# Optimization experiments

Hardware: AMD Instinct MI355X
Metric: run time of the kernel (lower is better)

Reference implementation:

```python
import jax, jax.numpy as jnp
import numpy as np

B, C, N, D = 8, 64, 512, 64

def setup_inputs() -> dict:
    key = jax.random.key(0)
    k1, = jax.random.split(key, 1)
    inp = jax.random.normal(k1, (B, C, N, D), dtype=jnp.float32)
    a = jnp.full((1, C, 1, 1), 0.75, dtype=jnp.float32)
    b = jnp.full((1, C, 1, 1), 0.25, dtype=jnp.float32)
    return {"inp": inp, "a": a, "b": b}

def reference(inp, a, b):
    # A = inp @ inp^T : [B, C, N, N]
    A = jnp.einsum('bcnd,bcmd->bcnm', inp, inp)
    # B = A @ A : [B, C, N, N]
    B2 = jnp.einsum('bcnk,bckm->bcnm', A, A)
    Mat = -a * A + b * B2
    # out = inp + Mat @ inp : [B, C, N, D]
    out = inp + jnp.einsum('bcnm,bcmd->bcnd', Mat, inp)
    return out
```

## Files before the change

### kernel.cpp

```cpp
#include <hip/hip_runtime.h>


typedef __bf16 bf16;
typedef __attribute__((ext_vector_type(8)))  __bf16 bf16x8;
typedef __attribute__((ext_vector_type(4)))  __bf16 bf16x4;
typedef __attribute__((ext_vector_type(16))) float  f32x16;

namespace {

constexpr int DD = 64;

__device__ __forceinline__ int sxz(int d) { return ((d >> 1) ^ (d >> 4)) & 7; }

__global__ __launch_bounds__(512, 4)
void ns_mfma(const float* __restrict__ inp, const float* __restrict__ aw,
             const float* __restrict__ bw, float* __restrict__ out) {
    __shared__ unsigned char smem[54272] __attribute__((aligned(128)));
    bf16*  const Xt0 = (bf16*)smem;
    bf16*  const Xt1 = (bf16*)(smem + 9216);
    bf16*  const Xr  = (bf16*)smem;
    float* const Gp  = (float*)(smem + 18432);
    bf16*  const Gbf = (bf16*)(smem + 35840);
    bf16*  const Hbf = (bf16*)(smem + 45056);

    const int slice = blockIdx.x;
    const float av = aw[slice & 63];
    const float bv = bw[slice & 63];
    const float* __restrict__ X = inp + (size_t)slice * (512 * DD);
    float* __restrict__ O       = out + (size_t)slice * (512 * DD);

    const int t    = threadIdx.x;
    const int lane = t & 63;
    const int w    = t >> 6;
    const int l31  = lane & 31;
    const int l5   = lane >> 5;
    const int half = t >> 8;
    const int th   = t & 255;
    const int s_nq = th >> 4;
    const int s_dq = th & 15;

    bf16x4 xr[4][4];
    {
        float4 rv[4][4];
#pragma unroll
        for (int s = 0; s < 4; ++s)
#pragma unroll
            for (int rn = 0; rn < 4; ++rn)
                rv[s][rn] = *(const float4*)&X[(256 * half + 64 * s + 4 * s_nq + rn) * DD + 4 * s_dq];
#pragma unroll
        for (int s = 0; s < 4; ++s)
#pragma unroll
            for (int rn = 0; rn < 4; ++rn) {
                xr[s][rn][0] = (bf16)rv[s][rn].x;
                xr[s][rn][1] = (bf16)rv[s][rn].y;
                xr[s][rn][2] = (bf16)rv[s][rn].z;
                xr[s][rn][3] = (bf16)rv[s][rn].w;
            }
    }

    f32x16 acc;
#pragma unroll
    for (int q = 0; q < 16; ++q) acc[q] = 0.f;

    bf16* const XtMine = half ? Xt1 : Xt0;
    const int tile = w & 3;
    const int i32  = (tile >> 1) * 32;
    const int j32  = (tile & 1) * 32;
    const int rowA = i32 + l31;
    const int rowB = j32 + l31;
    const int sA   = sxz(rowA);
    const int sB   = sxz(rowB);

    for (int it = 0; it < 4; ++it) {
#pragma unroll
        for (int r = 0; r < 4; ++r) {
            const int d = 4 * s_dq + r;
            bf16x4 v;
            v[0] = xr[it][0][r]; v[1] = xr[it][1][r];
            v[2] = xr[it][2][r]; v[3] = xr[it][3][r];
            const int g = ((s_nq >> 1) ^ sxz(d)) & 7;
            *(bf16x4*)&XtMine[d * 72 + g * 8 + 4 * (s_nq & 1)] = v;
        }
        __syncthreads();
#pragma unroll
        for (int ks = 0; ks < 4; ++ks) {
            const int gw = 2 * ks + l5;
            bf16x8 a = *(const bf16x8*)&XtMine[rowA * 72 + ((gw ^ sA) & 7) * 8];
            bf16x8 b = *(const bf16x8*)&XtMine[rowB * 72 + ((gw ^ sB) & 7) * 8];
            acc = __builtin_amdgcn_mfma_f32_32x32x16_bf16(a, b, acc, 0, 0, 0);
        }
        __syncthreads();
    }

    if (half == 0) {
#pragma unroll
        for (int q = 0; q < 16; ++q) {
            const int r = (q & 3) + 8 * (q >> 2) + 4 * l5;
            Gp[(i32 + r) * 68 + j32 + l31] = acc[q];
        }
    }
    __syncthreads();
    if (half == 1) {
#pragma unroll
        for (int q = 0; q < 16; ++q) {
            const int r  = (q & 3) + 8 * (q >> 2) + 4 * l5;
            const int ii = i32 + r;
            const int jj = j32 + l31;
            Gbf[ii * 72 + jj] = (bf16)(acc[q] + Gp[ii * 68 + jj]);
        }
    }
    __syncthreads();

    if (w < 4) {
        const int pi = (w >> 1) * 32;
        const int pj = (w & 1) * 32;
        f32x16 h;
#pragma unroll
        for (int q = 0; q < 16; ++q) h[q] = 0.f;
#pragma unroll
        for (int ks = 0; ks < 4; ++ks) {
            bf16x8 a = *(const bf16x8*)&Gbf[(pi + l31) * 72 + ks * 16 + 8 * l5];
            bf16x8 b = *(const bf16x8*)&Gbf[(pj + l31) * 72 + ks * 16 + 8 * l5];
            h = __builtin_amdgcn_mfma_f32_32x32x16_bf16(a, b, h, 0, 0, 0);
        }
#pragma unroll
        for (int q = 0; q < 16; ++q) {
            const int r  = (q & 3) + 8 * (q >> 2) + 4 * l5;
            const int ii = pi + r;
            const int jj = pj + l31;
            Hbf[ii * 72 + jj] = (bf16)(bv * h[q] - av * (float)Gbf[ii * 72 + jj]);
        }
    }
    __syncthreads();

    const int nb = (w >> 1) * 32;
    const int db = (w & 1) * 32;

    for (int it = 0; it < 4; ++it) {
        if (half == (it >> 1)) {
#pragma unroll
            for (int ss = 0; ss < 2; ++ss) {
                const int s   = 2 * (it & 1) + ss;
                const int nlb = 64 * ss + 4 * s_nq;
#pragma unroll
                for (int rn = 0; rn < 4; ++rn)
                    *(bf16x4*)&Xr[(nlb + rn) * 72 + 4 * s_dq] = xr[s][rn];
            }
        }
        __syncthreads();

        f32x16 o;
#pragma unroll
        for (int q = 0; q < 16; ++q) o[q] = 0.f;
#pragma unroll
        for (int ks = 0; ks < 4; ++ks) {
            bf16x8 a = *(const bf16x8*)&Xr [(nb + l31) * 72 + ks * 16 + 8 * l5];
            bf16x8 b = *(const bf16x8*)&Hbf[(db + l31) * 72 + ks * 16 + 8 * l5];
            o = __builtin_amdgcn_mfma_f32_32x32x16_bf16(a, b, o, 0, 0, 0);
        }

#pragma unroll
        for (int q = 0; q < 16; ++q) {
            const int rl = (q & 3) + 8 * (q >> 2) + 4 * l5;
            const int nl = nb + rl;
            const int d  = db + l31;
            O[(size_t)(it * 128 + nl) * DD + d] = o[q] + (float)Xr[nl * 72 + d];
        }
        __syncthreads();
    }
}

}

extern "C" void kernel_launch(void* const* d_in, const int* in_sizes, int n_in,
                              void* d_out, int out_size, void* d_ws, size_t ws_size,
                              hipStream_t stream) {
    const float* inp = (const float*)d_in[0];
    const float* aw  = (const float*)d_in[1];
    const float* bw  = (const float*)d_in[2];
    float* out       = (float*)d_out;

    ns_mfma<<<dim3(512), dim3(512), 0, stream>>>(inp, aw, bw, out);
}
```

Measured before the change: 25.61 us.

## Stream input chunks with double-buffered prefetch and reorder row ownership

Input rows are now loaded 128 at a time, with the next chunk prefetched into a two-slot float4 buffer while the current chunk is converted to bf16 and fed to the Gram MFMA loop. This replaces the upfront load of all 16 float4 per thread. Row ownership changes so both thread halves contribute to every 128-row chunk. The first output chunk is staged into shared memory during the Gram reduction, and one barrier per output iteration is removed. The goal is to overlap global-load latency with compute and lower peak register use, at the cost of more interleaved load and barrier logic.

```diff
diff --git a/kernel.cpp b/kernel.cpp
--- a/kernel.cpp
+++ b/kernel.cpp
@@ -7,8 +7,6 @@
 typedef __attribute__((ext_vector_type(16))) float  f32x16;
 
 namespace {
-
-constexpr int DD = 64;
 
 __device__ __forceinline__ int sxz(int d) { return ((d >> 1) ^ (d >> 4)) & 7; }
 
@@ -24,10 +22,8 @@
     bf16*  const Hbf = (bf16*)(smem + 45056);
 
     const int slice = blockIdx.x;
-    const float av = aw[slice & 63];
-    const float bv = bw[slice & 63];
-    const float* __restrict__ X = inp + (size_t)slice * (512 * DD);
-    float* __restrict__ O       = out + (size_t)slice * (512 * DD);
+    const float* __restrict__ X = inp + (size_t)slice * (512 * 64);
+    float* __restrict__ O       = out + (size_t)slice * (512 * 64);
 
     const int t    = threadIdx.x;
     const int lane = t & 63;
@@ -39,24 +35,16 @@
     const int s_nq = th >> 4;
     const int s_dq = th & 15;
 
-    bf16x4 xr[4][4];
-    {
-        float4 rv[4][4];
+    const float* __restrict__ Xbase =
+        X + (size_t)(64 * half + 4 * s_nq) * 64 + 4 * s_dq;
+
+    float4 rv[2][4];
 #pragma unroll
-        for (int s = 0; s < 4; ++s)
-#pragma unroll
-            for (int rn = 0; rn < 4; ++rn)
-                rv[s][rn] = *(const float4*)&X[(256 * half + 64 * s + 4 * s_nq + rn) * DD + 4 * s_dq];
-#pragma unroll
-        for (int s = 0; s < 4; ++s)
-#pragma unroll
-            for (int rn = 0; rn < 4; ++rn) {
-                xr[s][rn][0] = (bf16)rv[s][rn].x;
-                xr[s][rn][1] = (bf16)rv[s][rn].y;
-                xr[s][rn][2] = (bf16)rv[s][rn].z;
-                xr[s][rn][3] = (bf16)rv[s][rn].w;
-            }
-    }
+    for (int rn = 0; rn < 4; ++rn)
+        rv[0][rn] = *(const float4*)&Xbase[(size_t)rn * 64];
+
+    const float av = aw[slice & 63];
+    const float bv = bw[slice & 63];
 
     f32x16 acc;
 #pragma unroll
@@ -71,7 +59,22 @@
     const int sA   = sxz(rowA);
     const int sB   = sxz(rowB);
 
+    bf16x4 xr[4][4];
+
+#pragma unroll
     for (int it = 0; it < 4; ++it) {
+        if (it < 3) {
+#pragma unroll
+            for (int rn = 0; rn < 4; ++rn)
+                rv[(it + 1) & 1][rn] =
+                    *(const float4*)&Xbase[(size_t)(128 * (it + 1) + rn) * 64];
+        }
+#pragma unroll
+        for (int rn = 0; rn < 4; ++rn) {
+            const float4 v = rv[it & 1][rn];
+            xr[it][rn][0] = (bf16)v.x; xr[it][rn][1] = (bf16)v.y;
+            xr[it][rn][2] = (bf16)v.z; xr[it][rn][3] = (bf16)v.w;
+        }
 #pragma unroll
         for (int r = 0; r < 4; ++r) {
             const int d = 4 * s_dq + r;
@@ -99,6 +102,9 @@
             Gp[(i32 + r) * 68 + j32 + l31] = acc[q];
         }
     }
+#pragma unroll
+    for (int rn = 0; rn < 4; ++rn)
+        *(bf16x4*)&Xr[(64 * half + 4 * s_nq + rn) * 72 + 4 * s_dq] = xr[0][rn];
     __syncthreads();
     if (half == 1) {
 #pragma unroll
@@ -136,19 +142,8 @@
     const int nb = (w >> 1) * 32;
     const int db = (w & 1) * 32;
 
+#pragma unroll
     for (int it = 0; it < 4; ++it) {
-        if (half == (it >> 1)) {
-#pragma unroll
-            for (int ss = 0; ss < 2; ++ss) {
-                const int s   = 2 * (it & 1) + ss;
-                const int nlb = 64 * ss + 4 * s_nq;
-#pragma unroll
-                for (int rn = 0; rn < 4; ++rn)
-                    *(bf16x4*)&Xr[(nlb + rn) * 72 + 4 * s_dq] = xr[s][rn];
-            }
-        }
-        __syncthreads();
-
         f32x16 o;
 #pragma unroll
         for (int q = 0; q < 16; ++q) o[q] = 0.f;
@@ -158,15 +153,20 @@
             bf16x8 b = *(const bf16x8*)&Hbf[(db + l31) * 72 + ks * 16 + 8 * l5];
             o = __builtin_amdgcn_mfma_f32_32x32x16_bf16(a, b, o, 0, 0, 0);
         }
-
 #pragma unroll
         for (int q = 0; q < 16; ++q) {
             const int rl = (q & 3) + 8 * (q >> 2) + 4 * l5;
             const int nl = nb + rl;
             const int d  = db + l31;
-            O[(size_t)(it * 128 + nl) * DD + d] = o[q] + (float)Xr[nl * 72 + d];
+            O[(size_t)(it * 128 + nl) * 64 + d] = o[q] + (float)Xr[nl * 72 + d];
         }
-        __syncthreads();
+        if (it < 3) {
+            __syncthreads();
+#pragma unroll
+            for (int rn = 0; rn < 4; ++rn)
+                *(bf16x4*)&Xr[(64 * half + 4 * s_nq + rn) * 72 + 4 * s_dq] = xr[it + 1][rn];
+            __syncthreads();
+        }
     }
 }
 
```

Result: slower. 26.57 us (+3.8%).

## Double-buffer LDS staging tiles to halve barriers in Gram and output phases

Applied to the files above, without the earlier changes.

Each half of the block now gets two ping-pong LDS buffers for its transposed X tile, which removes the trailing barrier in each Gram accumulation step. The half assignment is inverted so the half holding the first 256 rows stages its row-major X tiles into two Xr buffers while the other half writes its partial Gram. The output loop then alternates between Xr0 and Xr1, filling the next buffer while the current one is consumed, with one barrier per step instead of two. In exchange, shared memory grows to about 71 KB and the launch-bounds occupancy hint drops from 4 to 2, which gives the compiler more registers but may lower residency.

```diff
diff --git a/kernel.cpp b/kernel.cpp
--- a/kernel.cpp
+++ b/kernel.cpp
@@ -8,26 +8,21 @@
 
 namespace {
 
-constexpr int DD = 64;
-
 __device__ __forceinline__ int sxz(int d) { return ((d >> 1) ^ (d >> 4)) & 7; }
 
-__global__ __launch_bounds__(512, 4)
+__global__ __launch_bounds__(512, 2)
 void ns_mfma(const float* __restrict__ inp, const float* __restrict__ aw,
              const float* __restrict__ bw, float* __restrict__ out) {
-    __shared__ unsigned char smem[54272] __attribute__((aligned(128)));
-    bf16*  const Xt0 = (bf16*)smem;
-    bf16*  const Xt1 = (bf16*)(smem + 9216);
-    bf16*  const Xr  = (bf16*)smem;
-    float* const Gp  = (float*)(smem + 18432);
-    bf16*  const Gbf = (bf16*)(smem + 35840);
-    bf16*  const Hbf = (bf16*)(smem + 45056);
+    __shared__ unsigned char smem[72704] __attribute__((aligned(128)));
+    float* const Gp  = (float*)(smem + 36864);
+    bf16*  const Gbf = (bf16*)(smem + 54272);
+    bf16*  const Hbf = (bf16*)(smem + 63488);
+    bf16*  const Xr0 = (bf16*)smem;
+    bf16*  const Xr1 = (bf16*)(smem + 18432);
 
     const int slice = blockIdx.x;
-    const float av = aw[slice & 63];
-    const float bv = bw[slice & 63];
-    const float* __restrict__ X = inp + (size_t)slice * (512 * DD);
-    float* __restrict__ O       = out + (size_t)slice * (512 * DD);
+    const float* __restrict__ X = inp + (size_t)slice * 32768;
+    float* __restrict__ O       = out + (size_t)slice * 32768;
 
     const int t    = threadIdx.x;
     const int lane = t & 63;
@@ -39,6 +34,9 @@
     const int s_nq = th >> 4;
     const int s_dq = th & 15;
 
+    const float* __restrict__ Xbase =
+        X + (size_t)(256 * (1 - half) + 4 * s_nq) * 64 + 4 * s_dq;
+
     bf16x4 xr[4][4];
     {
         float4 rv[4][4];
@@ -46,7 +44,7 @@
         for (int s = 0; s < 4; ++s)
 #pragma unroll
             for (int rn = 0; rn < 4; ++rn)
-                rv[s][rn] = *(const float4*)&X[(256 * half + 64 * s + 4 * s_nq + rn) * DD + 4 * s_dq];
+                rv[s][rn] = *(const float4*)&Xbase[(size_t)(64 * s + rn) * 64];
 #pragma unroll
         for (int s = 0; s < 4; ++s)
 #pragma unroll
@@ -57,12 +55,13 @@
                 xr[s][rn][3] = (bf16)rv[s][rn].w;
             }
     }
+    const float av = aw[slice & 63];
+    const float bv = bw[slice & 63];
 
     f32x16 acc;
 #pragma unroll
     for (int q = 0; q < 16; ++q) acc[q] = 0.f;
 
-    bf16* const XtMine = half ? Xt1 : Xt0;
     const int tile = w & 3;
     const int i32  = (tile >> 1) * 32;
     const int j32  = (tile & 1) * 32;
@@ -71,7 +70,11 @@
     const int sA   = sxz(rowA);
     const int sB   = sxz(rowB);
 
+    unsigned char* const XtH = smem + half * 18432;
+
+#pragma unroll
     for (int it = 0; it < 4; ++it) {
+        bf16* const Xt = (bf16*)(XtH + (it & 1) * 9216);
 #pragma unroll
         for (int r = 0; r < 4; ++r) {
             const int d = 4 * s_dq + r;
@@ -79,24 +82,33 @@
             v[0] = xr[it][0][r]; v[1] = xr[it][1][r];
             v[2] = xr[it][2][r]; v[3] = xr[it][3][r];
             const int g = ((s_nq >> 1) ^ sxz(d)) & 7;
-            *(bf16x4*)&XtMine[d * 72 + g * 8 + 4 * (s_nq & 1)] = v;
+            *(bf16x4*)&Xt[d * 72 + g * 8 + 4 * (s_nq & 1)] = v;
         }
         __syncthreads();
 #pragma unroll
         for (int ks = 0; ks < 4; ++ks) {
             const int gw = 2 * ks + l5;
-            bf16x8 a = *(const bf16x8*)&XtMine[rowA * 72 + ((gw ^ sA) & 7) * 8];
-            bf16x8 b = *(const bf16x8*)&XtMine[rowB * 72 + ((gw ^ sB) & 7) * 8];
+            bf16x8 a = *(const bf16x8*)&Xt[rowA * 72 + ((gw ^ sA) & 7) * 8];
+            bf16x8 b = *(const bf16x8*)&Xt[rowB * 72 + ((gw ^ sB) & 7) * 8];
             acc = __builtin_amdgcn_mfma_f32_32x32x16_bf16(a, b, acc, 0, 0, 0);
         }
-        __syncthreads();
     }
+    __syncthreads();
 
     if (half == 0) {
 #pragma unroll
         for (int q = 0; q < 16; ++q) {
             const int r = (q & 3) + 8 * (q >> 2) + 4 * l5;
             Gp[(i32 + r) * 68 + j32 + l31] = acc[q];
+        }
+    } else {
+#pragma unroll
+        for (int s = 0; s < 4; ++s) {
+            bf16* const Xr = (s >> 1) ? Xr1 : Xr0;
+            const int rowbase = 64 * (s & 1) + 4 * s_nq;
+#pragma unroll
+            for (int rn = 0; rn < 4; ++rn)
+                *(bf16x4*)&Xr[(rowbase + rn) * 72 + 4 * s_dq] = xr[s][rn];
         }
     }
     __syncthreads();
@@ -136,18 +148,21 @@
     const int nb = (w >> 1) * 32;
     const int db = (w & 1) * 32;
 
-    for (int it = 0; it < 4; ++it) {
-        if (half == (it >> 1)) {
+#pragma unroll
+    for (int tt = 0; tt < 4; ++tt) {
+        if (tt > 0) __syncthreads();
+        if (half == 0 && (tt == 1 || tt == 2)) {
+            bf16* const Xr = ((tt + 1) & 1) ? Xr1 : Xr0;
 #pragma unroll
             for (int ss = 0; ss < 2; ++ss) {
-                const int s   = 2 * (it & 1) + ss;
-                const int nlb = 64 * ss + 4 * s_nq;
+                const int s       = 2 * (tt - 1) + ss;
+                const int rowbase = 64 * ss + 4 * s_nq;
 #pragma unroll
                 for (int rn = 0; rn < 4; ++rn)
-                    *(bf16x4*)&Xr[(nlb + rn) * 72 + 4 * s_dq] = xr[s][rn];
+                    *(bf16x4*)&Xr[(rowbase + rn) * 72 + 4 * s_dq] = xr[s][rn];
             }
         }
-        __syncthreads();
+        const bf16* const Xr = (tt & 1) ? Xr1 : Xr0;
 
         f32x16 o;
 #pragma unroll
@@ -158,15 +173,13 @@
             bf16x8 b = *(const bf16x8*)&Hbf[(db + l31) * 72 + ks * 16 + 8 * l5];
             o = __builtin_amdgcn_mfma_f32_32x32x16_bf16(a, b, o, 0, 0, 0);
         }
-
 #pragma unroll
         for (int q = 0; q < 16; ++q) {
             const int rl = (q & 3) + 8 * (q >> 2) + 4 * l5;
             const int nl = nb + rl;
             const int d  = db + l31;
-            O[(size_t)(it * 128 + nl) * DD + d] = o[q] + (float)Xr[nl * 72 + d];
+            O[(size_t)(tt * 128 + nl) * 64 + d] = o[q] + (float)Xr[nl * 72 + d];
         }
-        __syncthreads();
     }
 }
 
```

New measurement: 25.40 us, median of 2. No clear change (-0.8%).
